# Kernel optimization log

Hardware: AMD Instinct MI355X
Metric: run time of the kernel (lower is better)

The kernel has to match this reference:

```python
import jax, jax.numpy as jnp
import numpy as np
import math

N, KZ, IFZ, AHZ, AFZ = 2048, 20, 128, 4, 32
LN_EPS = 1e-5


def setup_inputs() -> dict:
    key = jax.random.key(0)
    ks = jax.random.split(key, 8)
    s = 1.0 / math.sqrt(IFZ)
    return {
        "x_2": jax.random.normal(ks[0], (N, KZ, IFZ), jnp.float32),
        "edge_index": jax.random.randint(ks[1], (N, KZ), 0, N, dtype=jnp.int64),
        "Wq": jax.random.normal(ks[2], (IFZ, AHZ * AFZ), jnp.float32) * s,
        "Wk": jax.random.normal(ks[3], (IFZ, AHZ * AFZ), jnp.float32) * s,
        "Wv": jax.random.normal(ks[4], (IFZ, AHZ * AFZ), jnp.float32) * s,
        "Wb": jax.random.normal(ks[5], (IFZ, AHZ), jnp.float32) * s,
        "Wg": jax.random.normal(ks[6], (IFZ, AHZ * AFZ), jnp.float32) * s,
        "bg": jnp.zeros((AHZ * AFZ,), jnp.float32),
        "Wback": jax.random.normal(ks[7], (AHZ * AFZ, IFZ), jnp.float32) * s,
        "bback": jnp.zeros((IFZ,), jnp.float32),
        "gamma": jnp.ones((IFZ,), jnp.float32),
        "beta": jnp.zeros((IFZ,), jnp.float32),
    }


def _edge_attention(x_2, edge_index, Wq, Wk, Wv, Wb, Wg, bg, Wback, bback, gamma, beta):
    n, kz, _ = x_2.shape
    ahz, afz = AHZ, AFZ
    # projections: [N, kz, ahz, afz]
    q = (x_2 @ Wq).reshape(n, kz, ahz, afz)
    k = (x_2 @ Wk).reshape(n, kz, ahz, afz)
    v = (x_2 @ Wv).reshape(n, kz, ahz, afz)
    gate = jax.nn.sigmoid((x_2 @ Wg + bg).reshape(n, kz, ahz, afz))
    b = x_2 @ Wb  # [N, kz, ahz]
    scale = math.sqrt(afz)
    # neighbor gathers: [N, kz, kz, ahz, afz] (dominant memory traffic)
    k_nb = k[edge_index]
    v_nb = v[edge_index]
    b_nb = b[edge_index]  # [N, kz, kz, ahz]
    # self part: key[edge_temp][n,i,j] == k[n,j] -> avoid materializing broadcast
    s_self = jnp.einsum('nkac,njac->nkja', q, k) / scale + b[:, None, :, :]
    s_nb = jnp.einsum('nkac,nkjac->nkja', q, k_nb) / scale + b_nb
    scores = jnp.concatenate([s_self, s_nb], axis=2)  # [N, kz, 2kz, ahz]
    w = jax.nn.softmax(scores, axis=2)
    w_self, w_nb = w[:, :, :kz], w[:, :, kz:]
    ctx = (jnp.einsum('nkja,njac->nkac', w_self, v)
           + jnp.einsum('nkja,nkjac->nkac', w_nb, v_nb))
    out = gate * ctx  # [N, kz, ahz, afz]
    back = out.reshape(n, kz, ahz * afz) @ Wback + bback
    y = back + math.sqrt(2.0) * x_2
    mu = jnp.mean(y, axis=-1, keepdims=True)
    var = jnp.mean((y - mu) ** 2, axis=-1, keepdims=True)
    return gamma * (y - mu) / jnp.sqrt(var + LN_EPS) + beta


def reference(x_2, edge_index, Wq, Wk, Wv, Wb, Wg, bg, Wback, bback, gamma, beta):
    return _edge_attention(x_2, edge_index, Wq, Wk, Wv, Wb, Wg, bg, Wback, bback, gamma, beta)
```

## Files before the change

kernel.cpp:

```cpp
#include <hip/hip_runtime.h>
#include <math.h>

#define NN   2048
#define KZ   20
#define IFZ  128
#define AHZ  4
#define AFZ  32
#define ROWS (NN*KZ)
#define TWO_KZ (2*KZ)

typedef __attribute__((ext_vector_type(8))) short short8v;
typedef __attribute__((ext_vector_type(4))) float f32x4;
typedef __attribute__((ext_vector_type(2))) float f32x2;

__device__ __forceinline__ float blo(unsigned int u) {
    union { unsigned int i; float f; } x; x.i = u << 16; return x.f;
}
__device__ __forceinline__ float bhi(unsigned int u) {
    union { unsigned int i; float f; } x; x.i = u & 0xffff0000u; return x.f;
}
__device__ __forceinline__ unsigned short f2b(float f) {
    union { float f; unsigned int i; } x; x.f = f;
    unsigned int r = x.i + 0x7fffu + ((x.i >> 16) & 1u);
    return (unsigned short)(r >> 16);
}
__device__ __forceinline__ unsigned pack2(float a, float b) {
    return (unsigned)f2b(a) | ((unsigned)f2b(b) << 16);
}
__device__ __forceinline__ float dotf8_16(uint4 q, uint4 k) {
    float s = 0.f;
    f32x2 ql, qh, kl, kh;
    ql = __builtin_amdgcn_cvt_pk_f32_fp8(q.x, false); qh = __builtin_amdgcn_cvt_pk_f32_fp8(q.x, true);
    kl = __builtin_amdgcn_cvt_pk_f32_fp8(k.x, false); kh = __builtin_amdgcn_cvt_pk_f32_fp8(k.x, true);
    s += ql.x*kl.x + ql.y*kl.y + qh.x*kh.x + qh.y*kh.y;
    ql = __builtin_amdgcn_cvt_pk_f32_fp8(q.y, false); qh = __builtin_amdgcn_cvt_pk_f32_fp8(q.y, true);
    kl = __builtin_amdgcn_cvt_pk_f32_fp8(k.y, false); kh = __builtin_amdgcn_cvt_pk_f32_fp8(k.y, true);
    s += ql.x*kl.x + ql.y*kl.y + qh.x*kh.x + qh.y*kh.y;
    ql = __builtin_amdgcn_cvt_pk_f32_fp8(q.z, false); qh = __builtin_amdgcn_cvt_pk_f32_fp8(q.z, true);
    kl = __builtin_amdgcn_cvt_pk_f32_fp8(k.z, false); kh = __builtin_amdgcn_cvt_pk_f32_fp8(k.z, true);
    s += ql.x*kl.x + ql.y*kl.y + qh.x*kh.x + qh.y*kh.y;
    ql = __builtin_amdgcn_cvt_pk_f32_fp8(q.w, false); qh = __builtin_amdgcn_cvt_pk_f32_fp8(q.w, true);
    kl = __builtin_amdgcn_cvt_pk_f32_fp8(k.w, false); kh = __builtin_amdgcn_cvt_pk_f32_fp8(k.w, true);
    s += ql.x*kl.x + ql.y*kl.y + qh.x*kh.x + qh.y*kh.y;
    return s;
}

__global__ __launch_bounds__(256) void setup_kernel(
    const float* __restrict__ x,
    const float* __restrict__ Wq, const float* __restrict__ Wk,
    const float* __restrict__ Wv, const float* __restrict__ Wg,
    const float* __restrict__ Wback, const float* __restrict__ Wb,
    unsigned short* __restrict__ Wt, unsigned short* __restrict__ Wbt,
    float* __restrict__ bbuf)
{
    const int b   = blockIdx.x;
    const int tid = threadIdx.x;

    if (b < 320) {
        const int gid = b * 256 + tid;
        if (gid < 512 * 128) {
            const int n = gid >> 7, k = gid & 127;
            const float* W; int c;
            if      (n < 128) { W = Wq; c = n; }
            else if (n < 256) { W = Wk; c = n - 128; }
            else if (n < 384) { W = Wv; c = n - 256; }
            else              { W = Wg; c = n - 384; }
            Wt[gid] = f2b(W[k * 128 + c]);
        } else {
            const int g2 = gid - 512 * 128;
            const int n = g2 >> 7, k = g2 & 127;
            Wbt[g2] = f2b(Wback[k * 128 + n]);
        }
    } else {
        const int row = (b - 320) * 256 + tid;
        const float4* xv = (const float4*)(x + (size_t)row * IFZ);
        const float4* wv = (const float4*)Wb;
        float4 acc = make_float4(0.f, 0.f, 0.f, 0.f);
        #pragma unroll
        for (int k4 = 0; k4 < 32; ++k4) {
            const float4 xc = xv[k4];
            float4 w;
            w = wv[k4*4+0]; acc.x += xc.x*w.x; acc.y += xc.x*w.y; acc.z += xc.x*w.z; acc.w += xc.x*w.w;
            w = wv[k4*4+1]; acc.x += xc.y*w.x; acc.y += xc.y*w.y; acc.z += xc.y*w.z; acc.w += xc.y*w.w;
            w = wv[k4*4+2]; acc.x += xc.z*w.x; acc.y += xc.z*w.y; acc.z += xc.z*w.z; acc.w += xc.z*w.w;
            w = wv[k4*4+3]; acc.x += xc.w*w.x; acc.y += xc.w*w.y; acc.z += xc.w*w.z; acc.w += xc.w*w.w;
        }
        ((float4*)bbuf)[row] = acc;
    }
}

__global__ __launch_bounds__(256) void proj_gemm(
    const float* __restrict__ x, const unsigned short* __restrict__ Wt,
    const float* __restrict__ bg,
    unsigned short* __restrict__ gb,
    unsigned char* __restrict__ qf8, unsigned char* __restrict__ kf8,
    unsigned char* __restrict__ vf8)
{
    const int row0 = blockIdx.x * 128;
    const int wid  = threadIdx.x >> 6;
    const int lane = threadIdx.x & 63;
    const int wm = wid >> 1, wn = wid & 1;
    const int l15 = lane & 15, lg = lane >> 4;

    short8v a[4][4];
    {
        const float* Af = x + ((size_t)(row0 + wm*64 + l15)) * IFZ + lg*8;
        #pragma unroll
        for (int ks = 0; ks < 4; ++ks)
            #pragma unroll
            for (int fm = 0; fm < 4; ++fm) {
                const float4 u0 = *(const float4*)(Af + (size_t)fm*16*IFZ + ks*32);
                const float4 u1 = *(const float4*)(Af + (size_t)fm*16*IFZ + ks*32 + 4);
                union { short8v s; uint4 u; } cv;
                cv.u.x = pack2(u0.x, u0.y);
                cv.u.y = pack2(u0.z, u0.w);
                cv.u.z = pack2(u1.x, u1.y);
                cv.u.w = pack2(u1.z, u1.w);
                a[ks][fm] = cv.s;
            }
    }

    #pragma unroll
    for (int cc = 0; cc < 4; ++cc) {
        const unsigned short* Bb = Wt + ((size_t)(cc*128 + wn*64 + l15)) * IFZ + lg*8;

        f32x4 acc[4][4];
        #pragma unroll
        for (int i = 0; i < 4; ++i)
            #pragma unroll
            for (int j = 0; j < 4; ++j) acc[i][j] = (f32x4){0.f,0.f,0.f,0.f};

        #pragma unroll
        for (int ks = 0; ks < 4; ++ks) {
            short8v b[4];
            #pragma unroll
            for (int f = 0; f < 4; ++f)
                b[f] = *((const short8v*)(Bb + (size_t)f*16*IFZ + ks*32));
            #pragma unroll
            for (int fm = 0; fm < 4; ++fm)
                #pragma unroll
                for (int fn = 0; fn < 4; ++fn)
                    acc[fm][fn] = __builtin_amdgcn_mfma_f32_16x16x32_bf16(
                        b[fn], a[ks][fm], acc[fm][fn], 0, 0, 0);
        }

        const bool gate = (cc == 3);
        unsigned short* ob = (cc == 3) ? gb : (unsigned short*)0;
        unsigned char*  f8 = (cc == 0) ? qf8 : (cc == 1) ? kf8 : (cc == 2) ? vf8 : (unsigned char*)0;

        #pragma unroll
        for (int fm = 0; fm < 4; ++fm) {
            const int row = row0 + wm*64 + fm*16 + l15;
            #pragma unroll
            for (int fn = 0; fn < 4; ++fn) {
                const int cbase = wn*64 + fn*16 + lg*4;
                float v0 = acc[fm][fn][0], v1 = acc[fm][fn][1];
                float v2 = acc[fm][fn][2], v3 = acc[fm][fn][3];
                if (gate) {
                    const float4 bg4 = *(const float4*)(bg + cbase);
                    v0 = 1.f/(1.f + __expf(-(v0 + bg4.x)));
                    v1 = 1.f/(1.f + __expf(-(v1 + bg4.y)));
                    v2 = 1.f/(1.f + __expf(-(v2 + bg4.z)));
                    v3 = 1.f/(1.f + __expf(-(v3 + bg4.w)));
                    uint2 o;
                    o.x = pack2(v0, v1);
                    o.y = pack2(v2, v3);
                    *(uint2*)(ob + (size_t)row * IFZ + cbase) = o;
                } else {
                    int p = __builtin_amdgcn_cvt_pk_fp8_f32(v0, v1, 0, false);
                    p     = __builtin_amdgcn_cvt_pk_fp8_f32(v2, v3, p, true);
                    *(unsigned*)(f8 + (size_t)row*128 + cbase) = (unsigned)p;
                }
            }
        }
    }
}

__global__ __launch_bounds__(256) void attn_back_ln(
    const unsigned short* __restrict__ gb,
    const float* __restrict__ bbuf, const int* __restrict__ edge,
    const unsigned char* __restrict__ qf8, const unsigned char* __restrict__ kf8,
    const unsigned char* __restrict__ vf8,
    const float* __restrict__ x, const unsigned short* __restrict__ Wbt,
    const float* __restrict__ bback, const float* __restrict__ gamma,
    const float* __restrict__ beta, float* __restrict__ out)
{
    const int n   = blockIdx.x;
    const int tid = threadIdx.x;

    __shared__ unsigned smemA[2176];
    __shared__ float    scys[3280];
    __shared__ float    bs[KZ*AHZ];
    __shared__ float    st2[KZ][2];
    __shared__ int      es[KZ];

    unsigned* qsu8 = smemA;
    unsigned* ksu8 = smemA + 720;
    unsigned* ctxb = smemA;

    const size_t base  = (size_t)n * (KZ*IFZ);
    const size_t base2 = base >> 1;

    {
        const uint4* qsrc = (const uint4*)(qf8 + (size_t)n*(KZ*128));
        const uint4* ksrc = (const uint4*)(kf8 + (size_t)n*(KZ*128));
        for (int i = tid; i < KZ*8; i += 256) {
            const int r = i >> 3, u8 = i & 7;
            const int d = r*36 + (u8 >> 1)*8 + (u8 & 1)*4;
            *(uint4*)&qsu8[d] = qsrc[i];
            *(uint4*)&ksu8[d] = ksrc[i];
        }
    }
    if (tid < KZ)      es[tid] = edge[n*KZ + tid];
    if (tid < KZ*AHZ)  bs[tid] = bbuf[(size_t)n*(KZ*AHZ) + tid];
    __syncthreads();

    const float rscale = 0.17677669529663687f;

    for (int it = tid; it < KZ*KZ*AHZ; it += 256) {
        const int a  = it & 3;
        const int j  = (it >> 2) % KZ;
        const int kk = it / (KZ*AHZ);
        const unsigned* qrow = &qsu8[kk*36 + a*8];
        const unsigned* krow = &ksu8[j*36 + a*8];
        const uint4 q0 = *(const uint4*)&qrow[0];
        const uint4 q1 = *(const uint4*)&qrow[4];
        const uint4 k0 = *(const uint4*)&krow[0];
        const uint4 k1 = *(const uint4*)&krow[4];
        const float s = dotf8_16(q0, k0) + dotf8_16(q1, k1);
        scys[(kk*4 + a)*41 + j] = s*rscale + bs[j*AHZ + a];
    }

    for (int it = tid; it < KZ*KZ*AHZ; it += 256) {
        const int a  = it & 3;
        const int jj = (it >> 2) % KZ;
        const int kk = it / (KZ*AHZ);
        const int e  = es[kk];
        const unsigned* qrow = &qsu8[kk*36 + a*8];
        const uint4 q0 = *(const uint4*)&qrow[0];
        const uint4 q1 = *(const uint4*)&qrow[4];
        const unsigned char* kp = kf8 + ((size_t)e*KZ + jj)*128 + a*32;
        const uint4 k0 = *(const uint4*)kp;
        const uint4 k1 = *(const uint4*)(kp + 16);
        const float s = dotf8_16(q0, k0) + dotf8_16(q1, k1);
        scys[(kk*4 + a)*41 + KZ + jj] = s*rscale + bbuf[((size_t)e*KZ + jj)*AHZ + a];
    }
    __syncthreads();

    if (tid < KZ*AHZ) {
        float* row = &scys[tid*41];
        float m = row[0];
        #pragma unroll
        for (int j = 1; j < TWO_KZ; ++j) m = fmaxf(m, row[j]);
        float ssum = 0.f;
        #pragma unroll
        for (int j = 0; j < TWO_KZ; ++j) { const float e = __expf(row[j]-m); row[j] = e; ssum += e; }
        const float inv = 1.f/ssum;
        #pragma unroll
        for (int j = 0; j < TWO_KZ; ++j) row[j] *= inv;
    }
    __syncthreads();

    {
        for (int i = tid; i < 12*68; i += 256) ctxb[20*68 + i] = 0u;

        const unsigned* gbu = (const unsigned*)gb;
        for (int it = tid; it < KZ*64; it += 256) {
            const int kk = it >> 6;
            const int c2 = it & 63;
            const int a  = c2 >> 4;
            const float* wrow = &scys[(kk*4 + a)*41];
            float acc0 = 0.f, acc1 = 0.f;
            const unsigned char* vself = vf8 + (size_t)n*(KZ*128) + c2*2;
            #pragma unroll
            for (int j = 0; j < KZ; ++j) {
                const unsigned u = *(const unsigned short*)(vself + j*128);
                const f32x2 v2 = __builtin_amdgcn_cvt_pk_f32_fp8(u, false);
                const float w = wrow[j];
                acc0 += w*v2.x; acc1 += w*v2.y;
            }
            const unsigned char* vnb = vf8 + (size_t)es[kk]*(KZ*128) + c2*2;
            #pragma unroll
            for (int j = 0; j < KZ; ++j) {
                const unsigned u = *(const unsigned short*)(vnb + j*128);
                const f32x2 v2 = __builtin_amdgcn_cvt_pk_f32_fp8(u, false);
                const float w = wrow[KZ + j];
                acc0 += w*v2.x; acc1 += w*v2.y;
            }
            const unsigned gu = gbu[base2 + it];
            ctxb[kk*68 + c2] = pack2(acc0 * blo(gu), acc1 * bhi(gu));
        }
    }
    __syncthreads();

    const int wid  = tid >> 6;
    const int lane = tid & 63;
    const int l15  = lane & 15, lg = lane >> 4;
    const float SQ2 = 1.4142135623730951f;

    f32x4 bacc[2][2];
    #pragma unroll
    for (int i = 0; i < 2; ++i)
        #pragma unroll
        for (int j = 0; j < 2; ++j) bacc[i][j] = (f32x4){0.f,0.f,0.f,0.f};

    #pragma unroll
    for (int ks = 0; ks < 4; ++ks) {
        short8v bfr[2], afr[2];
        #pragma unroll
        for (int fn = 0; fn < 2; ++fn)
            bfr[fn] = *((const short8v*)(Wbt + (size_t)(wid*32 + fn*16 + l15)*IFZ + ks*32 + lg*8));
        #pragma unroll
        for (int fm = 0; fm < 2; ++fm)
            afr[fm] = *((const short8v*)&ctxb[(fm*16 + l15)*68 + ks*16 + lg*4]);
        #pragma unroll
        for (int fm = 0; fm < 2; ++fm)
            #pragma unroll
            for (int fn = 0; fn < 2; ++fn)
                bacc[fm][fn] = __builtin_amdgcn_mfma_f32_16x16x32_bf16(
                    bfr[fn], afr[fm], bacc[fm][fn], 0, 0, 0);
    }

    for (int i = tid; i < 640; i += 256) {
        const int r = i >> 5, c4 = (i & 31) * 4;
        const float4 xv  = *(const float4*)(x + base + (size_t)r*IFZ + c4);
        const float4 bb4 = *(const float4*)(bback + c4);
        float* yp = &scys[r*132 + c4];
        yp[0] = SQ2*xv.x + bb4.x; yp[1] = SQ2*xv.y + bb4.y;
        yp[2] = SQ2*xv.z + bb4.z; yp[3] = SQ2*xv.w + bb4.w;
    }
    __syncthreads();

    #pragma unroll
    for (int fm = 0; fm < 2; ++fm) {
        const int row = fm*16 + l15;
        if (row < KZ) {
            #pragma unroll
            for (int fn = 0; fn < 2; ++fn) {
                const int cb = wid*32 + fn*16 + lg*4;
                float* yp = &scys[row*132 + cb];
                yp[0] += bacc[fm][fn][0]; yp[1] += bacc[fm][fn][1];
                yp[2] += bacc[fm][fn][2]; yp[3] += bacc[fm][fn][3];
            }
        }
    }
    __syncthreads();

    if (tid < 160) {
        const int row = tid >> 3, t = tid & 7;
        float s1 = 0.f, s2 = 0.f;
        #pragma unroll
        for (int i = 0; i < 16; ++i) {
            const float v = scys[row*132 + t*16 + i];
            s1 += v; s2 += v*v;
        }
        s1 += __shfl_xor(s1, 1); s2 += __shfl_xor(s2, 1);
        s1 += __shfl_xor(s1, 2); s2 += __shfl_xor(s2, 2);
        s1 += __shfl_xor(s1, 4); s2 += __shfl_xor(s2, 4);
        if (t == 0) {
            const float mean = s1 * (1.f/IFZ);
            const float var  = s2 * (1.f/IFZ) - mean*mean;
            st2[row][0] = mean;
            st2[row][1] = rsqrtf(var + 1e-5f);
        }
    }
    __syncthreads();

    for (int i = tid; i < 640; i += 256) {
        const int r = i >> 5, c4 = (i & 31) * 4;
        const float mean = st2[r][0], rstd = st2[r][1];
        const float4 g4 = *(const float4*)(gamma + c4);
        const float4 b4 = *(const float4*)(beta + c4);
        const float4 yv = *(const float4*)&scys[r*132 + c4];
        float4 o;
        o.x = g4.x*(yv.x - mean)*rstd + b4.x;
        o.y = g4.y*(yv.y - mean)*rstd + b4.y;
        o.z = g4.z*(yv.z - mean)*rstd + b4.z;
        o.w = g4.w*(yv.w - mean)*rstd + b4.w;
        *(float4*)(out + base + (size_t)r*IFZ + c4) = o;
    }
}

extern "C" void kernel_launch(void* const* d_in, const int* in_sizes, int n_in,
                              void* d_out, int out_size, void* d_ws, size_t ws_size,
                              hipStream_t stream) {
    const float* x     = (const float*)d_in[0];
    const int*   edge  = (const int*)  d_in[1];
    const float* Wq    = (const float*)d_in[2];
    const float* Wk    = (const float*)d_in[3];
    const float* Wv    = (const float*)d_in[4];
    const float* Wb    = (const float*)d_in[5];
    const float* Wg    = (const float*)d_in[6];
    const float* bg    = (const float*)d_in[7];
    const float* Wback = (const float*)d_in[8];
    const float* bback = (const float*)d_in[9];
    const float* gamma = (const float*)d_in[10];
    const float* beta  = (const float*)d_in[11];
    float* out = (float*)d_out;

    const size_t RE = (size_t)ROWS * IFZ;
    unsigned short* gb  = (unsigned short*)d_ws;
    unsigned short* Wt  = gb + RE;
    unsigned short* Wbt = Wt + 512*128;
    float*          bbuf= (float*)(Wbt + 128*128);
    unsigned char*  qf8 = (unsigned char*)(bbuf + (size_t)ROWS*4);
    unsigned char*  kf8 = qf8 + RE;
    unsigned char*  vf8 = kf8 + RE;

    setup_kernel<<<480, 256, 0, stream>>>(x, Wq, Wk, Wv, Wg, Wback, Wb,
                                          Wt, Wbt, bbuf);
    proj_gemm  <<<ROWS/128, 256, 0, stream>>>(x, Wt, bg, gb, qf8, kf8, vf8);
    attn_back_ln<<<NN, 256, 0, stream>>>(gb, bbuf, edge, qf8, kf8, vf8,
                                         x, Wbt, bback, gamma, beta, out);
}
```

Before: 95.32 us.

## Split projection GEMM and attention kernel across more blocks for parallelism

After: 111.9 us. 17.4% more time.

```diff
diff --git a/kernel.cpp b/kernel.cpp
--- a/kernel.cpp
+++ b/kernel.cpp
@@ -3,6 +3,7 @@
 
 #define NN   2048
 #define KZ   20
+#define KH   10
 #define IFZ  128
 #define AHZ  4
 #define AFZ  32
@@ -121,8 +122,9 @@
     }
 
     #pragma unroll
-    for (int cc = 0; cc < 4; ++cc) {
-        const unsigned short* Bb = Wt + ((size_t)(cc*128 + wn*64 + l15)) * IFZ + lg*8;
+    for (int cc = 0; cc < 2; ++cc) {
+        const int ccg = (int)blockIdx.y * 2 + cc;
+        const unsigned short* Bb = Wt + ((size_t)(ccg*128 + wn*64 + l15)) * IFZ + lg*8;
 
         f32x4 acc[4][4];
         #pragma unroll
@@ -144,9 +146,8 @@
                         b[fn], a[ks][fm], acc[fm][fn], 0, 0, 0);
         }
 
-        const bool gate = (cc == 3);
-        unsigned short* ob = (cc == 3) ? gb : (unsigned short*)0;
-        unsigned char*  f8 = (cc == 0) ? qf8 : (cc == 1) ? kf8 : (cc == 2) ? vf8 : (unsigned char*)0;
+        const bool gate = (ccg == 3);
+        unsigned char* f8 = (ccg == 0) ? qf8 : (ccg == 1) ? kf8 : (ccg == 2) ? vf8 : (unsigned char*)0;
 
         #pragma unroll
         for (int fm = 0; fm < 4; ++fm) {
@@ -165,7 +166,7 @@
                     uint2 o;
                     o.x = pack2(v0, v1);
                     o.y = pack2(v2, v3);
-                    *(uint2*)(ob + (size_t)row * IFZ + cbase) = o;
+                    *(uint2*)(gb + (size_t)row * IFZ + cbase) = o;
                 } else {
                     int p = __builtin_amdgcn_cvt_pk_fp8_f32(v0, v1, 0, false);
                     p     = __builtin_amdgcn_cvt_pk_fp8_f32(v2, v3, p, true);
@@ -185,39 +186,40 @@
     const float* __restrict__ bback, const float* __restrict__ gamma,
     const float* __restrict__ beta, float* __restrict__ out)
 {
-    const int n   = blockIdx.x;
+    const int n   = blockIdx.x >> 1;
+    const int kk0 = (blockIdx.x & 1) * KH;
     const int tid = threadIdx.x;
 
-    __shared__ unsigned smemA[2176];
-    __shared__ float    scys[3280];
+    __shared__ unsigned smemA[1088];
+    __shared__ float    scys[1640];
     __shared__ float    bs[KZ*AHZ];
-    __shared__ float    st2[KZ][2];
-    __shared__ int      es[KZ];
+    __shared__ float    st2[KH][2];
+    __shared__ int      es[KH];
 
     unsigned* qsu8 = smemA;
-    unsigned* ksu8 = smemA + 720;
+    unsigned* ksu8 = smemA + 360;
     unsigned* ctxb = smemA;
 
     const size_t base  = (size_t)n * (KZ*IFZ);
-    const size_t base2 = base >> 1;
+    const size_t base2 = (size_t)n * (KZ*64);
 
     {
         const uint4* qsrc = (const uint4*)(qf8 + (size_t)n*(KZ*128));
         const uint4* ksrc = (const uint4*)(kf8 + (size_t)n*(KZ*128));
-        for (int i = tid; i < KZ*8; i += 256) {
-            const int r = i >> 3, u8 = i & 7;
-            const int d = r*36 + (u8 >> 1)*8 + (u8 & 1)*4;
-            *(uint4*)&qsu8[d] = qsrc[i];
-            *(uint4*)&ksu8[d] = ksrc[i];
-        }
-    }
-    if (tid < KZ)      es[tid] = edge[n*KZ + tid];
+        if (tid < 80) {
+            *(uint4*)&qsu8[(tid >> 3)*36 + (tid & 7)*4] = qsrc[kk0*8 + tid];
+        } else if (tid < 240) {
+            const int i2 = tid - 80;
+            *(uint4*)&ksu8[(i2 >> 3)*36 + (i2 & 7)*4] = ksrc[i2];
+        }
+    }
+    if (tid < KH)      es[tid] = edge[n*KZ + kk0 + tid];
     if (tid < KZ*AHZ)  bs[tid] = bbuf[(size_t)n*(KZ*AHZ) + tid];
     __syncthreads();
 
     const float rscale = 0.17677669529663687f;
 
-    for (int it = tid; it < KZ*KZ*AHZ; it += 256) {
+    for (int it = tid; it < KH*KZ*AHZ; it += 256) {
         const int a  = it & 3;
         const int j  = (it >> 2) % KZ;
         const int kk = it / (KZ*AHZ);
@@ -231,7 +233,7 @@
         scys[(kk*4 + a)*41 + j] = s*rscale + bs[j*AHZ + a];
     }
 
-    for (int it = tid; it < KZ*KZ*AHZ; it += 256) {
+    for (int it = tid; it < KH*KZ*AHZ; it += 256) {
         const int a  = it & 3;
         const int jj = (it >> 2) % KZ;
         const int kk = it / (KZ*AHZ);
@@ -247,7 +249,7 @@
     }
     __syncthreads();
 
-    if (tid < KZ*AHZ) {
+    if (tid < KH*AHZ) {
         float* row = &scys[tid*41];
         float m = row[0];
         #pragma unroll
@@ -262,10 +264,10 @@
     __syncthreads();
 
     {
-        for (int i = tid; i < 12*68; i += 256) ctxb[20*68 + i] = 0u;
+        for (int i = tid; i < 6*68; i += 256) ctxb[KH*68 + i] = 0u;
 
         const unsigned* gbu = (const unsigned*)gb;
-        for (int it = tid; it < KZ*64; it += 256) {
+        for (int it = tid; it < KH*64; it += 256) {
             const int kk = it >> 6;
             const int c2 = it & 63;
             const int a  = c2 >> 4;
@@ -287,7 +289,7 @@
                 const float w = wrow[KZ + j];
                 acc0 += w*v2.x; acc1 += w*v2.y;
             }
-            const unsigned gu = gbu[base2 + it];
+            const unsigned gu = gbu[base2 + (kk0 + kk)*64 + c2];
             ctxb[kk*68 + c2] = pack2(acc0 * blo(gu), acc1 * bhi(gu));
         }
     }
@@ -298,32 +300,26 @@
     const int l15  = lane & 15, lg = lane >> 4;
     const float SQ2 = 1.4142135623730951f;
 
-    f32x4 bacc[2][2];
-    #pragma unroll
-    for (int i = 0; i < 2; ++i)
-        #pragma unroll
-        for (int j = 0; j < 2; ++j) bacc[i][j] = (f32x4){0.f,0.f,0.f,0.f};
+    f32x4 bacc[2];
+    bacc[0] = (f32x4){0.f,0.f,0.f,0.f};
+    bacc[1] = (f32x4){0.f,0.f,0.f,0.f};
 
     #pragma unroll
     for (int ks = 0; ks < 4; ++ks) {
-        short8v bfr[2], afr[2];
+        short8v bfr[2], afr;
         #pragma unroll
         for (int fn = 0; fn < 2; ++fn)
             bfr[fn] = *((const short8v*)(Wbt + (size_t)(wid*32 + fn*16 + l15)*IFZ + ks*32 + lg*8));
-        #pragma unroll
-        for (int fm = 0; fm < 2; ++fm)
-            afr[fm] = *((const short8v*)&ctxb[(fm*16 + l15)*68 + ks*16 + lg*4]);
-        #pragma unroll
-        for (int fm = 0; fm < 2; ++fm)
-            #pragma unroll
-            for (int fn = 0; fn < 2; ++fn)
-                bacc[fm][fn] = __builtin_amdgcn_mfma_f32_16x16x32_bf16(
-                    bfr[fn], afr[fm], bacc[fm][fn], 0, 0, 0);
-    }
-
-    for (int i = tid; i < 640; i += 256) {
+        afr = *((const short8v*)&ctxb[l15*68 + ks*16 + lg*4]);
+        #pragma unroll
+        for (int fn = 0; fn < 2; ++fn)
+            bacc[fn] = __builtin_amdgcn_mfma_f32_16x16x32_bf16(
+                bfr[fn], afr, bacc[fn], 0, 0, 0);
+    }
+
+    for (int i = tid; i < KH*32; i += 256) {
         const int r = i >> 5, c4 = (i & 31) * 4;
-        const float4 xv  = *(const float4*)(x + base + (size_t)r*IFZ + c4);
+        const float4 xv  = *(const float4*)(x + base + (size_t)(kk0 + r)*IFZ + c4);
         const float4 bb4 = *(const float4*)(bback + c4);
         float* yp = &scys[r*132 + c4];
         yp[0] = SQ2*xv.x + bb4.x; yp[1] = SQ2*xv.y + bb4.y;
@@ -331,22 +327,18 @@
     }
     __syncthreads();
 
-    #pragma unroll
-    for (int fm = 0; fm < 2; ++fm) {
-        const int row = fm*16 + l15;
-        if (row < KZ) {
-            #pragma unroll
-            for (int fn = 0; fn < 2; ++fn) {
-                const int cb = wid*32 + fn*16 + lg*4;
-                float* yp = &scys[row*132 + cb];
-                yp[0] += bacc[fm][fn][0]; yp[1] += bacc[fm][fn][1];
-                yp[2] += bacc[fm][fn][2]; yp[3] += bacc[fm][fn][3];
-            }
-        }
-    }
-    __syncthreads();
-
-    if (tid < 160) {
+    if (l15 < KH) {
+        #pragma unroll
+        for (int fn = 0; fn < 2; ++fn) {
+            const int cb = wid*32 + fn*16 + lg*4;
+            float* yp = &scys[l15*132 + cb];
+            yp[0] += bacc[fn][0]; yp[1] += bacc[fn][1];
+            yp[2] += bacc[fn][2]; yp[3] += bacc[fn][3];
+        }
+    }
+    __syncthreads();
+
+    if (tid < KH*8) {
         const int row = tid >> 3, t = tid & 7;
         float s1 = 0.f, s2 = 0.f;
         #pragma unroll
@@ -366,7 +358,7 @@
     }
     __syncthreads();
 
-    for (int i = tid; i < 640; i += 256) {
+    for (int i = tid; i < KH*32; i += 256) {
         const int r = i >> 5, c4 = (i & 31) * 4;
         const float mean = st2[r][0], rstd = st2[r][1];
         const float4 g4 = *(const float4*)(gamma + c4);
@@ -377,7 +369,7 @@
         o.y = g4.y*(yv.y - mean)*rstd + b4.y;
         o.z = g4.z*(yv.z - mean)*rstd + b4.z;
         o.w = g4.w*(yv.w - mean)*rstd + b4.w;
-        *(float4*)(out + base + (size_t)r*IFZ + c4) = o;
+        *(float4*)(out + base + (size_t)(kk0 + r)*IFZ + c4) = o;
     }
 }
 
@@ -409,7 +401,7 @@
 
     setup_kernel<<<480, 256, 0, stream>>>(x, Wq, Wk, Wv, Wg, Wback, Wb,
                                           Wt, Wbt, bbuf);
-    proj_gemm  <<<ROWS/128, 256, 0, stream>>>(x, Wt, bg, gb, qf8, kf8, vf8);
-    attn_back_ln<<<NN, 256, 0, stream>>>(gb, bbuf, edge, qf8, kf8, vf8,
-                                         x, Wbt, bback, gamma, beta, out);
-}
+    proj_gemm  <<<dim3(ROWS/128, 2), 256, 0, stream>>>(x, Wt, bg, gb, qf8, kf8, vf8);
+    attn_back_ln<<<NN*2, 256, 0, stream>>>(gb, bbuf, edge, qf8, kf8, vf8,
+                                           x, Wbt, bback, gamma, beta, out);
+}
```
